# Kernel optimization log

Hardware: AMD Instinct MI355X
Metric: run time of the kernel (lower is better)

The kernel has to match this reference:

```python
import jax, jax.numpy as jnp
import numpy as np

B, S, D = 4, 2048, 1024  # batch, seq_len, d_model (h=16 but unused due to source bug)


def setup_inputs() -> dict:
    key = jax.random.key(0)
    ks = jax.random.split(key, 12)
    scale = 1.0 / np.sqrt(D)
    return {
        "q": jax.random.normal(ks[0], (B, S, D), jnp.float32),
        "k": jax.random.normal(ks[1], (B, S, D), jnp.float32),
        "v": jax.random.normal(ks[2], (B, S, D), jnp.float32),
        "mask": jnp.ones((1, 1, S, S), dtype=bool),
        "Wq": jax.random.normal(ks[3], (D, D), jnp.float32) * scale,
        "bq": jnp.zeros((D,), jnp.float32),
        "Wk": jax.random.normal(ks[4], (D, D), jnp.float32) * scale,
        "bk": jnp.zeros((D,), jnp.float32),
        "Wv": jax.random.normal(ks[5], (D, D), jnp.float32) * scale,
        "bv": jnp.zeros((D,), jnp.float32),
        "Wo": jax.random.normal(ks[6], (D, D), jnp.float32) * scale,
        "bo": jnp.zeros((D,), jnp.float32),
    }


def reference(q, k, v, mask, Wq, bq, Wk, bk, Wv, bv, Wo, bo):
    # Faithful to source bugs: head split discarded (attention over full d_model),
    # mask discarded (masked_fill out-of-place), dropout=0 (identity).
    query = q @ Wq + bq  # [B,S,D]
    key = k @ Wk + bk
    value = v @ Wv + bv
    d_k = query.shape[-1]  # = d_model due to the bug
    scores = jnp.einsum('bqd,bkd->bqk', query, key) / jnp.sqrt(jnp.float32(d_k))
    attn = jax.nn.softmax(scores, axis=-1)  # [B,S,S]
    x = jnp.einsum('bqk,bkd->bqd', attn, value)  # [B,S,D]
    # source: x.transpose(1,2).contiguous().view(B,-1,D) -> layout permutation
    b, s, d = x.shape
    x = jnp.swapaxes(x, 1, 2).reshape(b, s, d)
    return x @ Wo + bo
```

## Files before the change

### kernel.cpp

```cpp
#include <hip/hip_runtime.h>
#include <hip/hip_bf16.h>
#include <stdint.h>

typedef __attribute__((ext_vector_type(8))) short short8;
typedef __attribute__((ext_vector_type(4))) float f32x4;
typedef __attribute__((ext_vector_type(16))) float f32x16;
typedef const __attribute__((address_space(1))) uint32_t* gas1_t;
typedef __attribute__((address_space(3))) uint32_t* las3_t;

__device__ __forceinline__ short f2bf(float f) {
  uint32_t u = __builtin_bit_cast(uint32_t, f);
  u += 0x7fffu + ((u >> 16) & 1u);
  return (short)(u >> 16);
}
__device__ __forceinline__ float bf2f(short s) {
  return __builtin_bit_cast(float, ((uint32_t)(uint16_t)s) << 16);
}

__global__ __launch_bounds__(256) void cvt_qkv_k(const float* __restrict__ q,
    const float* __restrict__ k, const float* __restrict__ v,
    short* __restrict__ dst) {
  const long long n = 8388608LL;
  const float* src = (blockIdx.z == 0) ? q : (blockIdx.z == 1) ? k : v;
  long long i = ((long long)blockIdx.x * 256 + threadIdx.x) * 8;
  float4 a = *(const float4*)(src + i);
  float4 b = *(const float4*)(src + i + 4);
  short8 o;
  o[0]=f2bf(a.x); o[1]=f2bf(a.y); o[2]=f2bf(a.z); o[3]=f2bf(a.w);
  o[4]=f2bf(b.x); o[5]=f2bf(b.y); o[6]=f2bf(b.z); o[7]=f2bf(b.w);
  *(short8*)(dst + (long long)blockIdx.z * n + i) = o;
}

__global__ __launch_bounds__(256) void bias_gather_k(const float* b0, const float* b1,
    const float* b2, const float* b3, float* __restrict__ dst) {
  int i = blockIdx.x * 256 + threadIdx.x;
  if (i >= 4096) return;
  int z = i >> 10, j = i & 1023;
  const float* s = (z==0)?b0:(z==1)?b1:(z==2)?b2:b3;
  dst[i] = s[j];
}

__global__ __launch_bounds__(256) void wt_cvt_k(const float* w0, const float* w1,
    const float* w2, const float* w3, short* __restrict__ dst) {
  __shared__ float t[32][33];
  const float* W = (blockIdx.z==0)?w0:(blockIdx.z==1)?w1:(blockIdx.z==2)?w2:w3;
  short* D = dst + (long long)blockIdx.z * 1048576LL;
  int n0 = blockIdx.x * 32, k0 = blockIdx.y * 32;
  int tx = threadIdx.x, ty = threadIdx.y;
  #pragma unroll
  for (int i = 0; i < 4; ++i)
    t[ty + 8*i][tx] = W[(long long)(k0 + ty + 8*i) * 1024 + n0 + tx];
  __syncthreads();
  #pragma unroll
  for (int i = 0; i < 4; ++i)
    D[(long long)(n0 + ty + 8*i) * 1024 + k0 + tx] = f2bf(t[tx][ty + 8*i]);
}

__global__ __launch_bounds__(256) void softmax_bf_k(short* __restrict__ SP) {
  short* sp = SP + (long long)blockIdx.x * 2048;
  const int t = threadIdx.x;
  short8 sv = *(const short8*)(sp + t*8);
  float v[8];
  #pragma unroll
  for (int j = 0; j < 8; ++j) v[j] = bf2f(sv[j]);
  float m = v[0];
  #pragma unroll
  for (int j = 1; j < 8; ++j) m = fmaxf(m, v[j]);
  #pragma unroll
  for (int off = 32; off > 0; off >>= 1) m = fmaxf(m, __shfl_down(m, off, 64));
  __shared__ float rmax[4], rsum[4];
  int wv = t >> 6, ln = t & 63;
  if (ln == 0) rmax[wv] = m;
  __syncthreads();
  m = fmaxf(fmaxf(rmax[0], rmax[1]), fmaxf(rmax[2], rmax[3]));
  float e[8], sum = 0.f;
  #pragma unroll
  for (int j = 0; j < 8; ++j) { e[j] = exp2f((v[j] - m) * 1.44269504f); sum += e[j]; }
  #pragma unroll
  for (int off = 32; off > 0; off >>= 1) sum += __shfl_down(sum, off, 64);
  if (ln == 0) rsum[wv] = sum;
  __syncthreads();
  float inv = 1.0f / (rsum[0] + rsum[1] + rsum[2] + rsum[3]);
  short8 o;
  #pragma unroll
  for (int j = 0; j < 8; ++j) o[j] = f2bf(e[j] * inv);
  *(short8*)(sp + t*8) = o;
}

#define MFMA16(d, a_, b_) d = __builtin_amdgcn_mfma_f32_16x16x32_bf16(a_, b_, d, 0, 0, 0)
#define MFMA32(d, a_, b_) d = __builtin_amdgcn_mfma_f32_32x32x16_bf16(a_, b_, d, 0, 0, 0)
#define LGKM0 do { asm volatile("s_waitcnt lgkmcnt(0)" ::: "memory"); \
                   __builtin_amdgcn_sched_barrier(0); } while (0)
#define XCD_DECODE(gxs_, gys_) \
  const int nwg = (int)gridDim.x; \
  const int wg = ((int)blockIdx.x & 7) * (nwg >> 3) + ((int)blockIdx.x >> 3); \
  const int bxi = wg & ((1 << (gxs_)) - 1); \
  const int byi = (wg >> (gxs_)) & ((1 << (gys_)) - 1); \
  const int z = wg >> ((gxs_) + (gys_));

template<int OUT_BF16>
__global__ __launch_bounds__(512, 2) void gemm8_k(const short* __restrict__ A,
    const short* __restrict__ Bt, void* __restrict__ Cv,
    const float* __restrict__ bias,
    int M, int N, int K, long long sA, long long sB, long long sC,
    long long sBias, float scale, int gxs, int gys)
{
  __shared__ __align__(16) short lds[2][2][256*64];
  XCD_DECODE(gxs, gys);
  A  += (long long)z * sA;
  Bt += (long long)z * sB;
  const int bm = byi * 256;
  const int bn = bxi * 256;
  const int tid  = threadIdx.x;
  const int w    = tid >> 6, lane = tid & 63;
  const int wr   = w >> 2,   wc   = w & 3;
  const int lr   = lane & 15, lk  = lane >> 4;

  const int rsw0 = ((lk    ) ^ (lr & 7)) * 8;
  const int rsw1 = ((lk + 4) ^ (lr & 7)) * 8;
  const int srow = w * 8 + (lane >> 3);
  const int swc  = ((lane & 7) ^ ((lane >> 3) & 7)) * 8;
  const short* gA[4]; const short* gB[4];
  #pragma unroll
  for (int i = 0; i < 4; ++i) {
    gA[i] = A  + (long long)(bm + i*64 + srow) * K + swc;
    gB[i] = Bt + (long long)(bn + i*64 + srow) * K + swc;
  }

  #define STG(buf, ab, i, kt) \
    __builtin_amdgcn_global_load_lds((gas1_t)(((ab) ? gB : gA)[i] + (long long)(kt)*64), \
        (las3_t)&lds[buf][ab][(i)*4096 + w*512], 16, 0, 0)
  #define RDA(buf, mi, ks) (*(const short8*)&lds[buf][0][(wr*128 + (mi)*16 + lr)*64 + ((ks) ? rsw1 : rsw0)])
  #define RDB(buf, ni, ks) (*(const short8*)&lds[buf][1][(wc*64  + (ni)*16 + lr)*64 + ((ks) ? rsw1 : rsw0)])

  f32x4 acc[8][4] = {};
  const int nt = K >> 6;

  #pragma unroll
  for (int i = 0; i < 4; ++i) STG(0, 0, i, 0);
  #pragma unroll
  for (int i = 0; i < 4; ++i) STG(0, 1, i, 0);
  STG(1, 0, 0, 1); STG(1, 0, 2, 1);
  STG(1, 1, 0, 1); STG(1, 1, 1, 1);
  STG(1, 1, 2, 1); STG(1, 1, 3, 1);
  asm volatile("s_waitcnt vmcnt(6)" ::: "memory");
  __builtin_amdgcn_s_barrier();

  for (int g = 0; g < nt; ++g) {
    const int b = g & 1, nb = b ^ 1;
    short8 aR[4][2], bR[4][2];
    #pragma unroll
    for (int mi = 0; mi < 4; ++mi) { aR[mi][0] = RDA(b, mi, 0); aR[mi][1] = RDA(b, mi, 1); }
    #pragma unroll
    for (int ni = 0; ni < 2; ++ni) { bR[ni][0] = RDB(b, ni, 0); bR[ni][1] = RDB(b, ni, 1); }
    if (g + 1 < nt) { STG(nb, 0, 1, g+1); STG(nb, 0, 3, g+1); }
    __builtin_amdgcn_s_barrier();
    LGKM0;
    __builtin_amdgcn_s_setprio(1);
    #pragma unroll
    for (int mi = 0; mi < 4; ++mi)
      #pragma unroll
      for (int ni = 0; ni < 2; ++ni) {
        MFMA16(acc[mi][ni], aR[mi][0], bR[ni][0]);
        MFMA16(acc[mi][ni], aR[mi][1], bR[ni][1]);
      }
    __builtin_amdgcn_s_setprio(0);
    __builtin_amdgcn_s_barrier();
    #pragma unroll
    for (int ni = 2; ni < 4; ++ni) { bR[ni][0] = RDB(b, ni, 0); bR[ni][1] = RDB(b, ni, 1); }
    if (g + 2 < nt) { STG(b, 0, 0, g+2); STG(b, 0, 2, g+2); }
    __builtin_amdgcn_s_barrier();
    LGKM0;
    __builtin_amdgcn_s_setprio(1);
    #pragma unroll
    for (int mi = 0; mi < 4; ++mi)
      #pragma unroll
      for (int ni = 2; ni < 4; ++ni) {
        MFMA16(acc[mi][ni], aR[mi][0], bR[ni][0]);
        MFMA16(acc[mi][ni], aR[mi][1], bR[ni][1]);
      }
    __builtin_amdgcn_s_setprio(0);
    __builtin_amdgcn_s_barrier();
    #pragma unroll
    for (int mi = 0; mi < 4; ++mi) { aR[mi][0] = RDA(b, mi+4, 0); aR[mi][1] = RDA(b, mi+4, 1); }
    if (g + 2 < nt) { STG(b, 1, 0, g+2); STG(b, 1, 1, g+2); }
    __builtin_amdgcn_s_barrier();
    LGKM0;
    __builtin_amdgcn_s_setprio(1);
    #pragma unroll
    for (int mi = 0; mi < 4; ++mi)
      #pragma unroll
      for (int ni = 0; ni < 2; ++ni) {
        MFMA16(acc[mi+4][ni], aR[mi][0], bR[ni][0]);
        MFMA16(acc[mi+4][ni], aR[mi][1], bR[ni][1]);
      }
    __builtin_amdgcn_s_setprio(0);
    __builtin_amdgcn_s_barrier();
    if (g + 2 < nt) { STG(b, 1, 2, g+2); STG(b, 1, 3, g+2); }
    __builtin_amdgcn_s_setprio(1);
    #pragma unroll
    for (int mi = 0; mi < 4; ++mi)
      #pragma unroll
      for (int ni = 2; ni < 4; ++ni) {
        MFMA16(acc[mi+4][ni], aR[mi][0], bR[ni][0]);
        MFMA16(acc[mi+4][ni], aR[mi][1], bR[ni][1]);
      }
    __builtin_amdgcn_s_setprio(0);
    if (g + 1 < nt) {
      if (g + 2 < nt) asm volatile("s_waitcnt vmcnt(6)" ::: "memory");
      else            asm volatile("s_waitcnt vmcnt(0)" ::: "memory");
    }
    __builtin_amdgcn_s_barrier();
  }

  const float* bz = bias ? (bias + (long long)z * sBias) : nullptr;
  #pragma unroll
  for (int mi = 0; mi < 8; ++mi) {
    const int row = bm + wr*128 + mi*16 + lk*4;
    #pragma unroll
    for (int ni = 0; ni < 4; ++ni) {
      const int col = bn + wc*64 + ni*16 + lr;
      const float bval = bz ? bz[col] : 0.f;
      #pragma unroll
      for (int r = 0; r < 4; ++r) {
        float val = acc[mi][ni][r] * scale + bval;
        if (OUT_BF16)
          ((short*)Cv)[(long long)z*sC + (long long)(row + r) * N + col] = f2bf(val);
        else
          ((float*)Cv)[(long long)z*sC + (long long)(row + r) * N + col] = val;
      }
    }
  }
  #undef STG
  #undef RDA
  #undef RDB
}

template<int OUT_BF16, int BIAS_ROW>
__global__ __launch_bounds__(512, 2) void gemm4_k(const short* __restrict__ A,
    const short* __restrict__ Bt, void* __restrict__ Cv,
    const float* __restrict__ bias,
    int K, int lda, int ldb, int ldc,
    long long sA, long long sB, long long sC, long long sBias,
    float scale, int gxs, int gys)
{
  __shared__ __align__(16) short lds[3][24576];
  XCD_DECODE(gxs, gys);
  A  += (long long)z * sA;
  Bt += (long long)z * sB;
  const int bm = byi * 256;
  const int bn = bxi * 128;
  const int tid  = threadIdx.x;
  const int w    = tid >> 6, lane = tid & 63;
  const int wr   = w >> 1,   wc   = w & 1;
  const int l31  = lane & 31, l5 = lane >> 5, rq = lane & 7;

  const int srow = w * 8 + (lane >> 3);
  const int swc  = ((lane & 7) ^ ((lane >> 3) & 7)) * 8;
  const short* gA[4]; const short* gB[2];
  #pragma unroll
  for (int i = 0; i < 4; ++i)
    gA[i] = A + (long long)(bm + i*64 + srow) * lda + swc;
  #pragma unroll
  for (int i = 0; i < 2; ++i)
    gB[i] = Bt + (long long)(bn + i*64 + srow) * ldb + swc;

  #define STGA(buf, i, kt) \
    __builtin_amdgcn_global_load_lds((gas1_t)(gA[i] + (long long)(kt)*64), \
        (las3_t)&lds[buf][(i)*4096 + w*512], 16, 0, 0)
  #define STGB(buf, i, kt) \
    __builtin_amdgcn_global_load_lds((gas1_t)(gB[i] + (long long)(kt)*64), \
        (las3_t)&lds[buf][16384 + (i)*4096 + w*512], 16, 0, 0)
  #define RDA32(buf, mi, ks) (*(const short8*)&lds[buf][(wr*64 + (mi)*32 + l31)*64 + ((((ks)*2 + l5) ^ rq))*8])
  #define RDB32(buf, ni, ks) (*(const short8*)&lds[buf][16384 + (wc*64 + (ni)*32 + l31)*64 + ((((ks)*2 + l5) ^ rq))*8])

  f32x16 acc[2][2] = {};
  const int nt = K >> 6;

  STGA(0, 0, 0); STGA(0, 2, 0); STGB(0, 0, 0);
  STGB(0, 1, 0); STGA(0, 1, 0); STGA(0, 3, 0);
  STGA(1, 0, 1); STGA(1, 2, 1); STGB(1, 0, 1);
  STGB(1, 1, 1); STGA(1, 1, 1); STGA(1, 3, 1);
  asm volatile("s_waitcnt vmcnt(6)" ::: "memory");
  __builtin_amdgcn_s_barrier();

  int b = 0, nb = 2;
  for (int g = 0; g < nt; ++g) {
    short8 aR[2][2], bR[2][2];
    #pragma unroll
    for (int mi = 0; mi < 2; ++mi) { aR[mi][0] = RDA32(b, mi, 0); aR[mi][1] = RDA32(b, mi, 1); }
    #pragma unroll
    for (int ni = 0; ni < 2; ++ni) { bR[ni][0] = RDB32(b, ni, 0); bR[ni][1] = RDB32(b, ni, 1); }
    if (g + 2 < nt) { STGA(nb, 0, g+2); STGA(nb, 2, g+2); STGB(nb, 0, g+2); }
    LGKM0;
    __builtin_amdgcn_s_setprio(1);
    #pragma unroll
    for (int mi = 0; mi < 2; ++mi)
      #pragma unroll
      for (int ni = 0; ni < 2; ++ni) {
        MFMA32(acc[mi][ni], aR[mi][0], bR[ni][0]);
        MFMA32(acc[mi][ni], aR[mi][1], bR[ni][1]);
      }
    __builtin_amdgcn_s_setprio(0);
    #pragma unroll
    for (int mi = 0; mi < 2; ++mi) { aR[mi][0] = RDA32(b, mi, 2); aR[mi][1] = RDA32(b, mi, 3); }
    #pragma unroll
    for (int ni = 0; ni < 2; ++ni) { bR[ni][0] = RDB32(b, ni, 2); bR[ni][1] = RDB32(b, ni, 3); }
    if (g + 2 < nt) { STGB(nb, 1, g+2); STGA(nb, 1, g+2); STGA(nb, 3, g+2); }
    LGKM0;
    __builtin_amdgcn_s_setprio(1);
    #pragma unroll
    for (int mi = 0; mi < 2; ++mi)
      #pragma unroll
      for (int ni = 0; ni < 2; ++ni) {
        MFMA32(acc[mi][ni], aR[mi][0], bR[ni][0]);
        MFMA32(acc[mi][ni], aR[mi][1], bR[ni][1]);
      }
    __builtin_amdgcn_s_setprio(0);
    if (g + 2 < nt)      asm volatile("s_waitcnt vmcnt(6)" ::: "memory");
    else if (g + 1 < nt) asm volatile("s_waitcnt vmcnt(0)" ::: "memory");
    __builtin_amdgcn_s_barrier();
    b  = (b  == 2) ? 0 : b  + 1;
    nb = (nb == 2) ? 0 : nb + 1;
  }

  const float* bz = bias;
  #pragma unroll
  for (int mi = 0; mi < 2; ++mi) {
    #pragma unroll
    for (int ni = 0; ni < 2; ++ni) {
      const int col = bn + wc*64 + ni*32 + l31;
      const float bcol = (bz && !BIAS_ROW) ? bz[(long long)z*sBias + col] : 0.f;
      #pragma unroll
      for (int r = 0; r < 16; ++r) {
        const int row = bm + wr*64 + mi*32 + (r&3) + 8*(r>>2) + 4*l5;
        float bval = BIAS_ROW ? bz[row] : bcol;
        float val = acc[mi][ni][r] * scale + bval;
        if (OUT_BF16)
          ((short*)Cv)[(long long)z*sC + (long long)row * ldc + col] = f2bf(val);
        else
          ((float*)Cv)[(long long)z*sC + (long long)row * ldc + col] = val;
      }
    }
  }
  #undef STGA
  #undef STGB
  #undef RDA32
  #undef RDB32
}

extern "C" void kernel_launch(void* const* d_in, const int* in_sizes, int n_in,
                              void* d_out, int out_size, void* d_ws, size_t ws_size,
                              hipStream_t stream) {
  const float* q  = (const float*)d_in[0];
  const float* k  = (const float*)d_in[1];
  const float* v  = (const float*)d_in[2];
  const float* Wq = (const float*)d_in[4];
  const float* bq = (const float*)d_in[5];
  const float* Wk = (const float*)d_in[6];
  const float* bk = (const float*)d_in[7];
  const float* Wv = (const float*)d_in[8];
  const float* bv = (const float*)d_in[9];
  const float* Wo = (const float*)d_in[10];
  const float* bo = (const float*)d_in[11];

  char* w = (char*)d_ws;
  short* Wt     = (short*)(w);
  float* biasb  = (float*)(w + 8388608);
  short* QKV    = (short*)(w + 8404992);
  short* qkvbf  = (short*)(w + 58736640);
  short* P      = (short*)(w + 58736640);
  short* Vt     = (short*)(w + 109068288);
  short* xt     = (short*)(w + 125845504);

  short* Qp = QKV;
  short* Kp = QKV + 8388608LL;
  short* vbf = qkvbf + 16777216LL;

  cvt_qkv_k<<<dim3(4096,1,3), 256, 0, stream>>>(q, k, v, qkvbf);
  bias_gather_k<<<dim3(16), 256, 0, stream>>>(bq, bk, bv, bo, biasb);
  wt_cvt_k<<<dim3(32,32,4), dim3(32,8), 0, stream>>>(Wq, Wk, Wv, Wo, Wt);

  gemm8_k<1><<<256, 512, 0, stream>>>(qkvbf, Wt, QKV, biasb,
      8192, 1024, 1024, 8388608LL, 1048576LL, 8388608LL, 1024LL, 1.0f, 2, 5);

  gemm4_k<1,1><<<256, 512, 0, stream>>>(Wt + 2097152LL, vbf, Vt, biasb + 2048,
      1024, 1024, 1024, 8192, 0LL, 0LL, 0LL, 0LL, 1.0f, 6, 2);

  gemm8_k<1><<<256, 512, 0, stream>>>(Qp, Kp, P, nullptr,
      2048, 2048, 1024, 2097152LL, 2097152LL, 4194304LL, 0LL, 0.03125f, 3, 3);

  softmax_bf_k<<<dim3(8192), 256, 0, stream>>>(P);

  gemm4_k<1,0><<<256, 512, 0, stream>>>(Vt, P, xt, nullptr,
      2048, 8192, 2048, 2048, 2048LL, 4194304LL, 2097152LL, 0LL, 1.0f, 4, 2);

  gemm4_k<0,0><<<256, 512, 0, stream>>>(xt, Wt + 3145728LL, (float*)d_out,
      biasb + 3072, 1024, 1024, 1024, 1024, 2097152LL, 0LL, 2097152LL, 0LL, 1.0f, 3, 3);
}
```

Before: 215.3 us.

## Replace 256x256 GEMM with 256x128 K32 triple-buffered kernel for QKV and scores

Replaces the 256x256-tile, K=64 double-buffered gemm8 kernel with a 256x128 tile using K=32 slices and a three-stage LDS ring, one barrier per iteration, and launch bounds allowing 4 blocks per CU. The QK projection and QK^T score GEMMs now launch 512 workgroups instead of 256, aiming for better CU coverage and more latency hiding through occupancy. In exchange, each tile reuses its loaded data less, issues more global traffic per FLOP and does more loop iterations, and the tighter register budget may cause spills.

```diff
diff --git a/kernel.cpp b/kernel.cpp
--- a/kernel.cpp
+++ b/kernel.cpp
@@ -99,124 +99,77 @@
   const int z = wg >> ((gxs_) + (gys_));
 
 template<int OUT_BF16>
-__global__ __launch_bounds__(512, 2) void gemm8_k(const short* __restrict__ A,
+__global__ __launch_bounds__(512, 4) void gemm4h_k(const short* __restrict__ A,
     const short* __restrict__ Bt, void* __restrict__ Cv,
     const float* __restrict__ bias,
-    int M, int N, int K, long long sA, long long sB, long long sC,
-    long long sBias, float scale, int gxs, int gys)
+    int K, int lda, int ldb, int ldc,
+    long long sA, long long sB, long long sC, long long sBias,
+    float scale, int gxs, int gys)
 {
-  __shared__ __align__(16) short lds[2][2][256*64];
+  __shared__ __align__(16) short lds[3][12288];
   XCD_DECODE(gxs, gys);
   A  += (long long)z * sA;
   Bt += (long long)z * sB;
   const int bm = byi * 256;
-  const int bn = bxi * 256;
+  const int bn = bxi * 128;
   const int tid  = threadIdx.x;
   const int w    = tid >> 6, lane = tid & 63;
-  const int wr   = w >> 2,   wc   = w & 3;
+  const int wr   = w >> 1,   wc   = w & 1;
   const int lr   = lane & 15, lk  = lane >> 4;
 
-  const int rsw0 = ((lk    ) ^ (lr & 7)) * 8;
-  const int rsw1 = ((lk + 4) ^ (lr & 7)) * 8;
-  const int srow = w * 8 + (lane >> 3);
-  const int swc  = ((lane & 7) ^ ((lane >> 3) & 7)) * 8;
-  const short* gA[4]; const short* gB[4];
-  #pragma unroll
-  for (int i = 0; i < 4; ++i) {
-    gA[i] = A  + (long long)(bm + i*64 + srow) * K + swc;
-    gB[i] = Bt + (long long)(bn + i*64 + srow) * K + swc;
-  }
-
-  #define STG(buf, ab, i, kt) \
-    __builtin_amdgcn_global_load_lds((gas1_t)(((ab) ? gB : gA)[i] + (long long)(kt)*64), \
-        (las3_t)&lds[buf][ab][(i)*4096 + w*512], 16, 0, 0)
-  #define RDA(buf, mi, ks) (*(const short8*)&lds[buf][0][(wr*128 + (mi)*16 + lr)*64 + ((ks) ? rsw1 : rsw0)])
-  #define RDB(buf, ni, ks) (*(const short8*)&lds[buf][1][(wc*64  + (ni)*16 + lr)*64 + ((ks) ? rsw1 : rsw0)])
-
-  f32x4 acc[8][4] = {};
-  const int nt = K >> 6;
-
-  #pragma unroll
-  for (int i = 0; i < 4; ++i) STG(0, 0, i, 0);
-  #pragma unroll
-  for (int i = 0; i < 4; ++i) STG(0, 1, i, 0);
-  STG(1, 0, 0, 1); STG(1, 0, 2, 1);
-  STG(1, 1, 0, 1); STG(1, 1, 1, 1);
-  STG(1, 1, 2, 1); STG(1, 1, 3, 1);
-  asm volatile("s_waitcnt vmcnt(6)" ::: "memory");
+  const int rsw  = (lk ^ ((lr >> 1) & 3)) * 8;
+  const int srow = w * 16 + (lane >> 2);
+  const int sg   = ((lane & 3) ^ ((lane >> 3) & 3)) * 8;
+  const short* gA[2]; const short* gB;
+  #pragma unroll
+  for (int h = 0; h < 2; ++h)
+    gA[h] = A + (long long)(bm + h*128 + srow) * lda + sg;
+  gB = Bt + (long long)(bn + srow) * ldb + sg;
+
+  #define STGAh(buf, h, kt) \
+    __builtin_amdgcn_global_load_lds((gas1_t)(gA[h] + (long long)(kt)*32), \
+        (las3_t)&lds[buf][(h)*4096 + w*512], 16, 0, 0)
+  #define STGBh(buf, kt) \
+    __builtin_amdgcn_global_load_lds((gas1_t)(gB + (long long)(kt)*32), \
+        (las3_t)&lds[buf][8192 + w*512], 16, 0, 0)
+  #define RDAh(buf, mi) (*(const short8*)&lds[buf][(wr*64 + (mi)*16 + lr)*32 + rsw])
+  #define RDBh(buf, ni) (*(const short8*)&lds[buf][8192 + (wc*64 + (ni)*16 + lr)*32 + rsw])
+
+  f32x4 acc[4][4] = {};
+  const int nt = K >> 5;
+
+  STGAh(0, 0, 0); STGAh(0, 1, 0); STGBh(0, 0);
+  STGAh(1, 0, 1); STGAh(1, 1, 1); STGBh(1, 1);
+  asm volatile("s_waitcnt vmcnt(3)" ::: "memory");
   __builtin_amdgcn_s_barrier();
 
+  int b = 0, nb = 2;
   for (int g = 0; g < nt; ++g) {
-    const int b = g & 1, nb = b ^ 1;
-    short8 aR[4][2], bR[4][2];
-    #pragma unroll
-    for (int mi = 0; mi < 4; ++mi) { aR[mi][0] = RDA(b, mi, 0); aR[mi][1] = RDA(b, mi, 1); }
-    #pragma unroll
-    for (int ni = 0; ni < 2; ++ni) { bR[ni][0] = RDB(b, ni, 0); bR[ni][1] = RDB(b, ni, 1); }
-    if (g + 1 < nt) { STG(nb, 0, 1, g+1); STG(nb, 0, 3, g+1); }
-    __builtin_amdgcn_s_barrier();
+    short8 aR[4], bR[4];
+    #pragma unroll
+    for (int mi = 0; mi < 4; ++mi) aR[mi] = RDAh(b, mi);
+    #pragma unroll
+    for (int ni = 0; ni < 4; ++ni) bR[ni] = RDBh(b, ni);
+    if (g + 2 < nt) { STGAh(nb, 0, g+2); STGAh(nb, 1, g+2); STGBh(nb, g+2); }
     LGKM0;
     __builtin_amdgcn_s_setprio(1);
     #pragma unroll
     for (int mi = 0; mi < 4; ++mi)
       #pragma unroll
-      for (int ni = 0; ni < 2; ++ni) {
-        MFMA16(acc[mi][ni], aR[mi][0], bR[ni][0]);
-        MFMA16(acc[mi][ni], aR[mi][1], bR[ni][1]);
-      }
+      for (int ni = 0; ni < 4; ++ni)
+        MFMA16(acc[mi][ni], aR[mi], bR[ni]);
     __builtin_amdgcn_s_setprio(0);
+    if (g + 2 < nt)      asm volatile("s_waitcnt vmcnt(3)" ::: "memory");
+    else if (g + 1 < nt) asm volatile("s_waitcnt vmcnt(0)" ::: "memory");
     __builtin_amdgcn_s_barrier();
-    #pragma unroll
-    for (int ni = 2; ni < 4; ++ni) { bR[ni][0] = RDB(b, ni, 0); bR[ni][1] = RDB(b, ni, 1); }
-    if (g + 2 < nt) { STG(b, 0, 0, g+2); STG(b, 0, 2, g+2); }
-    __builtin_amdgcn_s_barrier();
-    LGKM0;
-    __builtin_amdgcn_s_setprio(1);
-    #pragma unroll
-    for (int mi = 0; mi < 4; ++mi)
-      #pragma unroll
-      for (int ni = 2; ni < 4; ++ni) {
-        MFMA16(acc[mi][ni], aR[mi][0], bR[ni][0]);
-        MFMA16(acc[mi][ni], aR[mi][1], bR[ni][1]);
-      }
-    __builtin_amdgcn_s_setprio(0);
-    __builtin_amdgcn_s_barrier();
-    #pragma unroll
-    for (int mi = 0; mi < 4; ++mi) { aR[mi][0] = RDA(b, mi+4, 0); aR[mi][1] = RDA(b, mi+4, 1); }
-    if (g + 2 < nt) { STG(b, 1, 0, g+2); STG(b, 1, 1, g+2); }
-    __builtin_amdgcn_s_barrier();
-    LGKM0;
-    __builtin_amdgcn_s_setprio(1);
-    #pragma unroll
-    for (int mi = 0; mi < 4; ++mi)
-      #pragma unroll
-      for (int ni = 0; ni < 2; ++ni) {
-        MFMA16(acc[mi+4][ni], aR[mi][0], bR[ni][0]);
-        MFMA16(acc[mi+4][ni], aR[mi][1], bR[ni][1]);
-      }
-    __builtin_amdgcn_s_setprio(0);
-    __builtin_amdgcn_s_barrier();
-    if (g + 2 < nt) { STG(b, 1, 2, g+2); STG(b, 1, 3, g+2); }
-    __builtin_amdgcn_s_setprio(1);
-    #pragma unroll
-    for (int mi = 0; mi < 4; ++mi)
-      #pragma unroll
-      for (int ni = 2; ni < 4; ++ni) {
-        MFMA16(acc[mi+4][ni], aR[mi][0], bR[ni][0]);
-        MFMA16(acc[mi+4][ni], aR[mi][1], bR[ni][1]);
-      }
-    __builtin_amdgcn_s_setprio(0);
-    if (g + 1 < nt) {
-      if (g + 2 < nt) asm volatile("s_waitcnt vmcnt(6)" ::: "memory");
-      else            asm volatile("s_waitcnt vmcnt(0)" ::: "memory");
-    }
-    __builtin_amdgcn_s_barrier();
+    b  = (b  == 2) ? 0 : b  + 1;
+    nb = (nb == 2) ? 0 : nb + 1;
   }
 
   const float* bz = bias ? (bias + (long long)z * sBias) : nullptr;
   #pragma unroll
-  for (int mi = 0; mi < 8; ++mi) {
-    const int row = bm + wr*128 + mi*16 + lk*4;
+  for (int mi = 0; mi < 4; ++mi) {
+    const int row = bm + wr*64 + mi*16 + lk*4;
     #pragma unroll
     for (int ni = 0; ni < 4; ++ni) {
       const int col = bn + wc*64 + ni*16 + lr;
@@ -225,15 +178,16 @@
       for (int r = 0; r < 4; ++r) {
         float val = acc[mi][ni][r] * scale + bval;
         if (OUT_BF16)
-          ((short*)Cv)[(long long)z*sC + (long long)(row + r) * N + col] = f2bf(val);
+          ((short*)Cv)[(long long)z*sC + (long long)(row + r) * ldc + col] = f2bf(val);
         else
-          ((float*)Cv)[(long long)z*sC + (long long)(row + r) * N + col] = val;
+          ((float*)Cv)[(long long)z*sC + (long long)(row + r) * ldc + col] = val;
       }
     }
   }
-  #undef STG
-  #undef RDA
-  #undef RDB
+  #undef STGAh
+  #undef STGBh
+  #undef RDAh
+  #undef RDBh
 }
 
 template<int OUT_BF16, int BIAS_ROW>
@@ -381,14 +335,14 @@
   bias_gather_k<<<dim3(16), 256, 0, stream>>>(bq, bk, bv, bo, biasb);
   wt_cvt_k<<<dim3(32,32,4), dim3(32,8), 0, stream>>>(Wq, Wk, Wv, Wo, Wt);
 
-  gemm8_k<1><<<256, 512, 0, stream>>>(qkvbf, Wt, QKV, biasb,
-      8192, 1024, 1024, 8388608LL, 1048576LL, 8388608LL, 1024LL, 1.0f, 2, 5);
+  gemm4h_k<1><<<512, 512, 0, stream>>>(qkvbf, Wt, QKV, biasb,
+      1024, 1024, 1024, 1024, 8388608LL, 1048576LL, 8388608LL, 1024LL, 1.0f, 3, 5);
 
   gemm4_k<1,1><<<256, 512, 0, stream>>>(Wt + 2097152LL, vbf, Vt, biasb + 2048,
       1024, 1024, 1024, 8192, 0LL, 0LL, 0LL, 0LL, 1.0f, 6, 2);
 
-  gemm8_k<1><<<256, 512, 0, stream>>>(Qp, Kp, P, nullptr,
-      2048, 2048, 1024, 2097152LL, 2097152LL, 4194304LL, 0LL, 0.03125f, 3, 3);
+  gemm4h_k<1><<<512, 512, 0, stream>>>(Qp, Kp, P, nullptr,
+      1024, 1024, 1024, 2048, 2097152LL, 2097152LL, 4194304LL, 0LL, 0.03125f, 4, 3);
 
   softmax_bf_k<<<dim3(8192), 256, 0, stream>>>(P);
 
```

New measurement: 219.2 us. No clear change (+1.8%).
